# Performance work log

Hardware: AMD Instinct MI355X
Metric: run time of the kernel (lower is better)

The kernel has to match this reference:

```python
import jax, jax.numpy as jnp
import numpy as np

N = 100000   # nodes
E = 1200000  # edges
D = 64       # feature dim (in_channels == out_channels)


def gcn_layer(x, W, src, dst):
    # GCNConv(normalize=False, bias=False, aggr='add'):
    # linear transform then scatter-add of source messages into targets.
    h = x @ W                                            # [N, D]
    msg = h[src]                                         # [E, D] gather
    return jax.ops.segment_sum(msg, dst, num_segments=x.shape[0])  # [N, D]


def setup_inputs() -> dict:
    key = jax.random.key(0)
    ks = jax.random.split(key, 5)
    x = jax.random.normal(ks[0], (N, D), dtype=jnp.float32)
    edge_index = jax.random.randint(ks[1], (2, E), 0, N, dtype=jnp.int64)
    scale = 1.0 / np.sqrt(D).astype(np.float32)
    W0 = jax.random.normal(ks[2], (D, D), dtype=jnp.float32) * scale
    W1 = jax.random.normal(ks[3], (D, D), dtype=jnp.float32) * scale
    W2 = jax.random.normal(ks[4], (D, D), dtype=jnp.float32) * scale
    return {"x": x, "edge_index": edge_index, "W0": W0, "W1": W1, "W2": W2}


def reference(x, edge_index, W0, W1, W2):
    src = edge_index[0]  # messages flow source -> target (PyG default)
    dst = edge_index[1]
    # num_hop = 3 stacked convs; dropout p=0 and use_bn=False are no-ops.
    for W in (W0, W1, W2):
        x = gcn_layer(x, W, src, dst)
    return x
```

## Files before the change

### kernel.cpp

```cpp
#include <hip/hip_runtime.h>


#define GCN_D 64
#define SEGSHIFT 8
#define SEGROWS 256
#define MAXSEG 512
#define A_EPB 4096

typedef unsigned short ushort;

__device__ __forceinline__ float bf2f(ushort u) {
    union { unsigned u; float f; } c; c.u = ((unsigned)u) << 16; return c.f;
}
__device__ __forceinline__ ushort f2bf(float f) {
    union { float f; unsigned u; } c; c.f = f;
    const unsigned r = 0x7FFFu + ((c.u >> 16) & 1u);
    return (ushort)((c.u + r) >> 16);
}

__global__ __launch_bounds__(256) void k_wchain(const float* __restrict__ W0,
                                                const float* __restrict__ W1,
                                                const float* __restrict__ W2,
                                                float* __restrict__ Wc) {
    __shared__ float A[4096], B[4096], T[4096];
    const int t = threadIdx.x;
    for (int i = t; i < 1024; i += 256) {
        ((float4*)A)[i] = ((const float4*)W0)[i];
        ((float4*)B)[i] = ((const float4*)W1)[i];
    }
    __syncthreads();
#pragma unroll
    for (int g = 0; g < 4; ++g) {
        const int idx = t + 256 * g;
        const int r = idx >> 4, c4 = idx & 15;
        float4 acc = make_float4(0.f, 0.f, 0.f, 0.f);
#pragma unroll
        for (int k = 0; k < 64; ++k) {
            const float a = A[r * 64 + k];
            const float4 b = ((float4*)B)[k * 16 + c4];
            acc.x = fmaf(a, b.x, acc.x); acc.y = fmaf(a, b.y, acc.y);
            acc.z = fmaf(a, b.z, acc.z); acc.w = fmaf(a, b.w, acc.w);
        }
        ((float4*)T)[idx] = acc;
    }
    __syncthreads();
    for (int i = t; i < 1024; i += 256) ((float4*)B)[i] = ((const float4*)W2)[i];
    __syncthreads();
#pragma unroll
    for (int g = 0; g < 4; ++g) {
        const int idx = t + 256 * g;
        const int r = idx >> 4, c4 = idx & 15;
        float4 acc = make_float4(0.f, 0.f, 0.f, 0.f);
#pragma unroll
        for (int k = 0; k < 64; ++k) {
            const float a = T[r * 64 + k];
            const float4 b = ((float4*)B)[k * 16 + c4];
            acc.x = fmaf(a, b.x, acc.x); acc.y = fmaf(a, b.y, acc.y);
            acc.z = fmaf(a, b.z, acc.z); acc.w = fmaf(a, b.w, acc.w);
        }
        ((float4*)Wc)[idx] = acc;
    }
}

__global__ __launch_bounds__(256) void k_tobf(const float* __restrict__ X,
                                              ushort* __restrict__ B, long long n4) {
    const long long stride = (long long)gridDim.x * 256;
    for (long long i = blockIdx.x * 256ll + threadIdx.x; i < n4; i += stride) {
        const float4 v = ((const float4*)X)[i];
        ushort4 u;
        u.x = f2bf(v.x); u.y = f2bf(v.y); u.z = f2bf(v.z); u.w = f2bf(v.w);
        ((ushort4*)B)[i] = u;
    }
}

__global__ __launch_bounds__(256) void k_a0(const int* __restrict__ ei,
                                            int* __restrict__ ghist, int E) {
    __shared__ int h[MAXSEG];
    const int t = threadIdx.x;
    for (int i = t; i < MAXSEG; i += 256) h[i] = 0;
    __syncthreads();
    for (int e = blockIdx.x * 256 + t; e < E; e += gridDim.x * 256)
        atomicAdd(&h[ei[E + e] >> SEGSHIFT], 1);
    __syncthreads();
    for (int i = t; i < MAXSEG; i += 256) {
        const int c = h[i];
        if (c) atomicAdd(&ghist[i], c);
    }
}

__global__ __launch_bounds__(MAXSEG) void k_ascan(const int* __restrict__ ghist,
                                                  int* __restrict__ gOff,
                                                  int* __restrict__ gcur,
                                                  int* __restrict__ rp, int N, int E) {
    __shared__ int sd[MAXSEG];
    const int t = threadIdx.x;
    const int v = ghist[t];
    sd[t] = v; __syncthreads();
    for (int off = 1; off < MAXSEG; off <<= 1) {
        const int y = (t >= off) ? sd[t - off] : 0;
        __syncthreads();
        sd[t] += y;
        __syncthreads();
    }
    const int excl = sd[t] - v;
    gOff[t] = excl; gcur[t] = excl;
    if (t == MAXSEG - 1) gOff[MAXSEG] = sd[t];
    if (t == 0) rp[N] = E;
}

__global__ __launch_bounds__(512) void k_apart(const int* __restrict__ ei,
                                               int* __restrict__ gcur,
                                               uint2* __restrict__ ebuf, int E) {
    __shared__ int hist[MAXSEG], lofs[MAXSEG], cur[MAXSEG], gbase[MAXSEG];
    __shared__ uint2 stg[A_EPB];
    const int t = threadIdx.x;
    const int base = blockIdx.x * A_EPB;
    const int cnt = min(A_EPB, E - base);

    hist[t] = 0;
    __syncthreads();

    uint2 my[8]; int mb[8];
#pragma unroll
    for (int j = 0; j < 8; ++j) {
        const int i = t + j * 512;
        if (i < cnt) {
            const int e = base + i;
            const int s = ei[e];
            const int d = ei[E + e];
            my[j] = make_uint2((unsigned)s, (unsigned)d);
            mb[j] = d >> SEGSHIFT;
            atomicAdd(&hist[mb[j]], 1);
        } else mb[j] = -1;
    }
    __syncthreads();

    {
        const int v = hist[t];
        lofs[t] = v; __syncthreads();
        for (int off = 1; off < MAXSEG; off <<= 1) {
            const int y = (t >= off) ? lofs[t - off] : 0;
            __syncthreads();
            lofs[t] += y;
            __syncthreads();
        }
        const int excl = lofs[t] - v;
        __syncthreads();
        lofs[t] = excl; cur[t] = excl;
    }
    __syncthreads();

#pragma unroll
    for (int j = 0; j < 8; ++j) {
        if (mb[j] >= 0) {
            const int p = atomicAdd(&cur[mb[j]], 1);
            stg[p] = my[j];
        }
    }
    __syncthreads();

    {
        const int c = hist[t];
        gbase[t] = c ? atomicAdd(&gcur[t], c) : 0;
    }
    __syncthreads();

    for (int i = t; i < cnt; i += 512) {
        const uint2 pr = stg[i];
        const int b = (int)(pr.y >> SEGSHIFT);
        ebuf[(size_t)gbase[b] + (unsigned)(i - lofs[b])] = pr;
    }
}

__global__ __launch_bounds__(SEGROWS) void k_bplace(const uint2* __restrict__ ebuf,
                                                    const int* __restrict__ gOff,
                                                    int* __restrict__ rp,
                                                    int* __restrict__ cs, int N) {
    __shared__ int h[SEGROWS], ofs[SEGROWS];
    const int s = blockIdx.x;
    const int t = threadIdx.x;
    const int e0 = gOff[s];
    const int e1 = gOff[s + 1];

    h[t] = 0; __syncthreads();
    for (int e = e0 + t; e < e1; e += SEGROWS)
        atomicAdd(&h[ebuf[e].y & (SEGROWS - 1)], 1);
    __syncthreads();

    const int v = h[t];
    ofs[t] = v; __syncthreads();
    for (int off = 1; off < SEGROWS; off <<= 1) {
        const int y = (t >= off) ? ofs[t - off] : 0;
        __syncthreads();
        ofs[t] += y;
        __syncthreads();
    }
    const int excl = ofs[t] - v;
    const int r = s * SEGROWS + t;
    if (r < N) rp[r] = e0 + excl;
    __syncthreads();
    ofs[t] = excl;
    __syncthreads();

    for (int e = e0 + t; e < e1; e += SEGROWS) {
        const uint2 pr = ebuf[e];
        const int lr = (int)(pr.y & (SEGROWS - 1));
        const int p = atomicAdd(&ofs[lr], 1);
        cs[e0 + p] = (int)pr.x;
    }
}

__global__ __launch_bounds__(256) void k_aggc(const ushort* __restrict__ B,
                                              const int* __restrict__ rp,
                                              const int* __restrict__ cs,
                                              ushort* __restrict__ out, int N) {
    const int t = threadIdx.x;
    const int gw = (blockIdx.x * 256 + t) >> 6;
    const int lane = t & 63;
    const int q = lane >> 4;
    const int f4 = lane & 15;
    const int r = gw * 4 + q;
    if (r >= N) return;

    const int e0 = rp[r];
    const int e1 = rp[r + 1];
    const ushort4* Bv = (const ushort4*)B;

    float4 acc = make_float4(0.f, 0.f, 0.f, 0.f);
    int e = e0;
    for (; e + 3 < e1; e += 4) {
        const int s0 = cs[e], s1 = cs[e + 1], s2 = cs[e + 2], s3 = cs[e + 3];
        const ushort4 u0 = Bv[(size_t)s0 * 16 + f4];
        const ushort4 u1 = Bv[(size_t)s1 * 16 + f4];
        const ushort4 u2 = Bv[(size_t)s2 * 16 + f4];
        const ushort4 u3 = Bv[(size_t)s3 * 16 + f4];
        acc.x += bf2f(u0.x) + bf2f(u1.x) + bf2f(u2.x) + bf2f(u3.x);
        acc.y += bf2f(u0.y) + bf2f(u1.y) + bf2f(u2.y) + bf2f(u3.y);
        acc.z += bf2f(u0.z) + bf2f(u1.z) + bf2f(u2.z) + bf2f(u3.z);
        acc.w += bf2f(u0.w) + bf2f(u1.w) + bf2f(u2.w) + bf2f(u3.w);
    }
    for (; e < e1; ++e) {
        const ushort4 u = Bv[(size_t)cs[e] * 16 + f4];
        acc.x += bf2f(u.x); acc.y += bf2f(u.y);
        acc.z += bf2f(u.z); acc.w += bf2f(u.w);
    }
    ushort4 o;
    o.x = f2bf(acc.x); o.y = f2bf(acc.y); o.z = f2bf(acc.z); o.w = f2bf(acc.w);
    ((ushort4*)out)[(size_t)r * 16 + f4] = o;
}

__global__ __launch_bounds__(256) void gcn_gemm64b(const ushort* __restrict__ X,
                                                   const float* __restrict__ W,
                                                   float* __restrict__ H,
                                                   int nrows) {
    __shared__ float Wl[64 * 64];
    __shared__ float Xl[16][65];

    const int tid = threadIdx.x;
    for (int i = tid; i < 1024; i += 256) ((float4*)Wl)[i] = ((const float4*)W)[i];

    const int rowBase = blockIdx.x * 16;
    const int lr = tid >> 4;
    const int lc = tid & 15;
    const int grow = rowBase + lr;

    if (grow < nrows) {
        const ushort4 u = ((const ushort4*)X)[(size_t)grow * 16 + lc];
        Xl[lr][lc * 4 + 0] = bf2f(u.x);
        Xl[lr][lc * 4 + 1] = bf2f(u.y);
        Xl[lr][lc * 4 + 2] = bf2f(u.z);
        Xl[lr][lc * 4 + 3] = bf2f(u.w);
    }
    __syncthreads();

    float4 acc = make_float4(0.f, 0.f, 0.f, 0.f);
#pragma unroll
    for (int k = 0; k < 64; ++k) {
        const float xv = Xl[lr][k];
        const float4 w4 = ((const float4*)Wl)[k * 16 + lc];
        acc.x = fmaf(xv, w4.x, acc.x);
        acc.y = fmaf(xv, w4.y, acc.y);
        acc.z = fmaf(xv, w4.z, acc.z);
        acc.w = fmaf(xv, w4.w, acc.w);
    }
    if (grow < nrows) ((float4*)H)[(size_t)grow * 16 + lc] = acc;
}

__global__ __launch_bounds__(256) void gcn_gemm64(const float* __restrict__ X,
                                                  const float* __restrict__ W,
                                                  float* __restrict__ H,
                                                  int nrows) {
    __shared__ float Wl[64 * 64];
    __shared__ float Xl[16][65];
    const int tid = threadIdx.x;
    for (int i = tid; i < 1024; i += 256) ((float4*)Wl)[i] = ((const float4*)W)[i];
    const int rowBase = blockIdx.x * 16;
    const int lr = tid >> 4;
    const int lc = tid & 15;
    const int grow = rowBase + lr;
    if (grow < nrows) {
        float4 xv = ((const float4*)X)[(long long)grow * 16 + lc];
        Xl[lr][lc * 4 + 0] = xv.x; Xl[lr][lc * 4 + 1] = xv.y;
        Xl[lr][lc * 4 + 2] = xv.z; Xl[lr][lc * 4 + 3] = xv.w;
    }
    __syncthreads();
    float4 acc = make_float4(0.f, 0.f, 0.f, 0.f);
#pragma unroll
    for (int k = 0; k < 64; ++k) {
        const float xv = Xl[lr][k];
        const float4 w4 = ((const float4*)Wl)[k * 16 + lc];
        acc.x = fmaf(xv, w4.x, acc.x); acc.y = fmaf(xv, w4.y, acc.y);
        acc.z = fmaf(xv, w4.z, acc.z); acc.w = fmaf(xv, w4.w, acc.w);
    }
    if (grow < nrows) ((float4*)H)[(long long)grow * 16 + lc] = acc;
}

__global__ __launch_bounds__(256) void gcn_scatter(const float* __restrict__ H,
                                                   const int* __restrict__ ei,
                                                   float* __restrict__ out,
                                                   int nedges) {
    const long long t = (long long)blockIdx.x * 256 + threadIdx.x;
    const int e = (int)(t >> 4);
    if (e >= nedges) return;
    const int lc = (int)(t & 15);
    const int s = ei[e];
    const int d = ei[nedges + e];
    const float4 v = ((const float4*)H)[(long long)s * 16 + lc];
    float* o = out + (long long)d * GCN_D + lc * 4;
    atomicAdd(o + 0, v.x);
    atomicAdd(o + 1, v.y);
    atomicAdd(o + 2, v.z);
    atomicAdd(o + 3, v.w);
}

extern "C" void kernel_launch(void* const* d_in, const int* in_sizes, int n_in,
                              void* d_out, int out_size, void* d_ws, size_t ws_size,
                              hipStream_t stream) {
    const float* x  = (const float*)d_in[0];
    const int*   ei = (const int*)d_in[1];
    const float* W0 = (const float*)d_in[2];
    const float* W1 = (const float*)d_in[3];
    const float* W2 = (const float*)d_in[4];
    float* out = (float*)d_out;

    const int N_ = in_sizes[0] / GCN_D;
    const int E_ = in_sizes[1] / 2;
    const int NSEG = (N_ + SEGROWS - 1) >> SEGSHIFT;

    uintptr_t base = (uintptr_t)d_ws;
    ushort* B0 = (ushort*)base;
    const size_t bfBytes  = (size_t)N_ * GCN_D * 2;
    const size_t regBytes = bfBytes > (size_t)E_ * 8 ? bfBytes : (size_t)E_ * 8;
    ushort* B1   = (ushort*)(base + bfBytes);
    uint2*  ebuf = (uint2*)B1;
    int* rp    = (int*)(base + bfBytes + regBytes);
    int* gOff  = rp + (N_ + 2);
    int* ghist = gOff + (MAXSEG + 1);
    int* gcur  = ghist + MAXSEG;
    float* Wc  = (float*)(gcur + MAXSEG);
    int* cs    = (int*)(Wc + 4096);
    const size_t needed = ((uintptr_t)(cs + E_) - base);

    const int gemmBlocks = (N_ + 15) / 16;

    if (NSEG <= MAXSEG && ws_size >= needed) {
        k_wchain<<<1, 256, 0, stream>>>(W0, W1, W2, Wc);
        k_tobf<<<1024, 256, 0, stream>>>(x, B0, (long long)N_ * 16);
        hipMemsetAsync(ghist, 0, MAXSEG * 4, stream);
        k_a0<<<512, 256, 0, stream>>>(ei, ghist, E_);
        k_ascan<<<1, MAXSEG, 0, stream>>>(ghist, gOff, gcur, rp, N_, E_);
        k_apart<<<(E_ + A_EPB - 1) / A_EPB, 512, 0, stream>>>(ei, gcur, ebuf, E_);
        k_bplace<<<NSEG, SEGROWS, 0, stream>>>(ebuf, gOff, rp, cs, N_);

        const int aggBlocks = (N_ + 15) / 16;
        k_aggc<<<aggBlocks, 256, 0, stream>>>(B0, rp, cs, B1, N_);
        k_aggc<<<aggBlocks, 256, 0, stream>>>(B1, rp, cs, B0, N_);
        k_aggc<<<aggBlocks, 256, 0, stream>>>(B0, rp, cs, B1, N_);
        gcn_gemm64b<<<gemmBlocks, 256, 0, stream>>>(B1, Wc, out, N_);
    } else {
        float* h = (float*)d_ws;
        const int scatBlocks = (int)(((long long)E_ * 16 + 255) / 256);
        const int edgeBlocks = (E_ + 255) / 256;
        (void)edgeBlocks;
        const float* curAct = x;
        for (int l = 0; l < 3; ++l) {
            const float* Wl = (l == 0) ? W0 : (l == 1) ? W1 : W2;
            gcn_gemm64<<<gemmBlocks, 256, 0, stream>>>(curAct, Wl, h, N_);
            hipMemsetAsync(out, 0, (size_t)N_ * GCN_D * sizeof(float), stream);
            gcn_scatter<<<scatBlocks, 256, 0, stream>>>(h, ei, out, E_);
            curAct = out;
        }
    }
}
```

Measured before the change: 189.5 us.

## Fuse final aggregation with weight GEMM, pack edge pairs, unroll gathers

The last aggregation pass is merged with the dense 64x64 weight multiply, so the bf16 intermediate is no longer written out and read back by a separate GEMM kernel. Edge (src, dst) pairs in the partition buffer are packed into one 32-bit word (src<<8 | local row), which halves staging and buffer traffic. Because the destination is no longer stored, each element finds its bucket by binary search over the local offsets. The ghist memset is folded into the bf16 conversion kernel, and the gather loops are unrolled to 8 edges to keep more loads in flight. The packing only holds for N < 2^24, so a guard is added.

```diff
diff --git a/kernel.cpp b/kernel.cpp
--- a/kernel.cpp
+++ b/kernel.cpp
@@ -63,7 +63,11 @@
 }
 
 __global__ __launch_bounds__(256) void k_tobf(const float* __restrict__ X,
-                                              ushort* __restrict__ B, long long n4) {
+                                              ushort* __restrict__ B,
+                                              int* __restrict__ ghist, long long n4) {
+    if (blockIdx.x == 0) {
+        for (int i = threadIdx.x; i < MAXSEG; i += 256) ghist[i] = 0;
+    }
     const long long stride = (long long)gridDim.x * 256;
     for (long long i = blockIdx.x * 256ll + threadIdx.x; i < n4; i += stride) {
         const float4 v = ((const float4*)X)[i];
@@ -110,9 +114,9 @@
 
 __global__ __launch_bounds__(512) void k_apart(const int* __restrict__ ei,
                                                int* __restrict__ gcur,
-                                               uint2* __restrict__ ebuf, int E) {
+                                               unsigned* __restrict__ ebuf, int E) {
     __shared__ int hist[MAXSEG], lofs[MAXSEG], cur[MAXSEG], gbase[MAXSEG];
-    __shared__ uint2 stg[A_EPB];
+    __shared__ unsigned stg[A_EPB];
     const int t = threadIdx.x;
     const int base = blockIdx.x * A_EPB;
     const int cnt = min(A_EPB, E - base);
@@ -120,16 +124,16 @@
     hist[t] = 0;
     __syncthreads();
 
-    uint2 my[8]; int mb[8];
+    unsigned my[8]; int mb[8];
 #pragma unroll
     for (int j = 0; j < 8; ++j) {
         const int i = t + j * 512;
         if (i < cnt) {
             const int e = base + i;
-            const int s = ei[e];
-            const int d = ei[E + e];
-            my[j] = make_uint2((unsigned)s, (unsigned)d);
-            mb[j] = d >> SEGSHIFT;
+            const unsigned s = (unsigned)ei[e];
+            const unsigned d = (unsigned)ei[E + e];
+            my[j] = (s << 8) | (d & (SEGROWS - 1));
+            mb[j] = (int)(d >> SEGSHIFT);
             atomicAdd(&hist[mb[j]], 1);
         } else mb[j] = -1;
     }
@@ -166,13 +170,16 @@
     __syncthreads();
 
     for (int i = t; i < cnt; i += 512) {
-        const uint2 pr = stg[i];
-        const int b = (int)(pr.y >> SEGSHIFT);
-        ebuf[(size_t)gbase[b] + (unsigned)(i - lofs[b])] = pr;
-    }
-}
-
-__global__ __launch_bounds__(SEGROWS) void k_bplace(const uint2* __restrict__ ebuf,
+        int lo = 0, hi = MAXSEG - 1;
+        while (lo < hi) {
+            const int mid = (lo + hi + 1) >> 1;
+            if (lofs[mid] <= i) lo = mid; else hi = mid - 1;
+        }
+        ebuf[(size_t)gbase[lo] + (unsigned)(i - lofs[lo])] = stg[i];
+    }
+}
+
+__global__ __launch_bounds__(SEGROWS) void k_bplace(const unsigned* __restrict__ ebuf,
                                                     const int* __restrict__ gOff,
                                                     int* __restrict__ rp,
                                                     int* __restrict__ cs, int N) {
@@ -184,7 +191,7 @@
 
     h[t] = 0; __syncthreads();
     for (int e = e0 + t; e < e1; e += SEGROWS)
-        atomicAdd(&h[ebuf[e].y & (SEGROWS - 1)], 1);
+        atomicAdd(&h[ebuf[e] & (SEGROWS - 1)], 1);
     __syncthreads();
 
     const int v = h[t];
@@ -203,10 +210,10 @@
     __syncthreads();
 
     for (int e = e0 + t; e < e1; e += SEGROWS) {
-        const uint2 pr = ebuf[e];
-        const int lr = (int)(pr.y & (SEGROWS - 1));
+        const unsigned pr = ebuf[e];
+        const int lr = (int)(pr & (SEGROWS - 1));
         const int p = atomicAdd(&ofs[lr], 1);
-        cs[e0 + p] = (int)pr.x;
+        cs[e0 + p] = (int)(pr >> 8);
     }
 }
 
@@ -217,9 +224,8 @@
     const int t = threadIdx.x;
     const int gw = (blockIdx.x * 256 + t) >> 6;
     const int lane = t & 63;
-    const int q = lane >> 4;
     const int f4 = lane & 15;
-    const int r = gw * 4 + q;
+    const int r = gw * 4 + (lane >> 4);
     if (r >= N) return;
 
     const int e0 = rp[r];
@@ -228,16 +234,25 @@
 
     float4 acc = make_float4(0.f, 0.f, 0.f, 0.f);
     int e = e0;
+    for (; e + 7 < e1; e += 8) {
+        ushort4 u[8];
+#pragma unroll
+        for (int j = 0; j < 8; ++j) u[j] = Bv[(size_t)cs[e + j] * 16 + f4];
+#pragma unroll
+        for (int j = 0; j < 8; ++j) {
+            acc.x += bf2f(u[j].x); acc.y += bf2f(u[j].y);
+            acc.z += bf2f(u[j].z); acc.w += bf2f(u[j].w);
+        }
+    }
     for (; e + 3 < e1; e += 4) {
-        const int s0 = cs[e], s1 = cs[e + 1], s2 = cs[e + 2], s3 = cs[e + 3];
-        const ushort4 u0 = Bv[(size_t)s0 * 16 + f4];
-        const ushort4 u1 = Bv[(size_t)s1 * 16 + f4];
-        const ushort4 u2 = Bv[(size_t)s2 * 16 + f4];
-        const ushort4 u3 = Bv[(size_t)s3 * 16 + f4];
-        acc.x += bf2f(u0.x) + bf2f(u1.x) + bf2f(u2.x) + bf2f(u3.x);
-        acc.y += bf2f(u0.y) + bf2f(u1.y) + bf2f(u2.y) + bf2f(u3.y);
-        acc.z += bf2f(u0.z) + bf2f(u1.z) + bf2f(u2.z) + bf2f(u3.z);
-        acc.w += bf2f(u0.w) + bf2f(u1.w) + bf2f(u2.w) + bf2f(u3.w);
+        ushort4 u[4];
+#pragma unroll
+        for (int j = 0; j < 4; ++j) u[j] = Bv[(size_t)cs[e + j] * 16 + f4];
+#pragma unroll
+        for (int j = 0; j < 4; ++j) {
+            acc.x += bf2f(u[j].x); acc.y += bf2f(u[j].y);
+            acc.z += bf2f(u[j].z); acc.w += bf2f(u[j].w);
+        }
     }
     for (; e < e1; ++e) {
         const ushort4 u = Bv[(size_t)cs[e] * 16 + f4];
@@ -249,41 +264,67 @@
     ((ushort4*)out)[(size_t)r * 16 + f4] = o;
 }
 
-__global__ __launch_bounds__(256) void gcn_gemm64b(const ushort* __restrict__ X,
-                                                   const float* __restrict__ W,
-                                                   float* __restrict__ H,
-                                                   int nrows) {
+__global__ __launch_bounds__(256) void k_aggf(const ushort* __restrict__ B,
+                                              const int* __restrict__ rp,
+                                              const int* __restrict__ cs,
+                                              const float* __restrict__ Wc,
+                                              float* __restrict__ out, int N) {
     __shared__ float Wl[64 * 64];
     __shared__ float Xl[16][65];
-
-    const int tid = threadIdx.x;
-    for (int i = tid; i < 1024; i += 256) ((float4*)Wl)[i] = ((const float4*)W)[i];
-
-    const int rowBase = blockIdx.x * 16;
-    const int lr = tid >> 4;
-    const int lc = tid & 15;
-    const int grow = rowBase + lr;
-
-    if (grow < nrows) {
-        const ushort4 u = ((const ushort4*)X)[(size_t)grow * 16 + lc];
-        Xl[lr][lc * 4 + 0] = bf2f(u.x);
-        Xl[lr][lc * 4 + 1] = bf2f(u.y);
-        Xl[lr][lc * 4 + 2] = bf2f(u.z);
-        Xl[lr][lc * 4 + 3] = bf2f(u.w);
-    }
-    __syncthreads();
+    const int t = threadIdx.x;
+    for (int i = t; i < 1024; i += 256) ((float4*)Wl)[i] = ((const float4*)Wc)[i];
+
+    const int lr = t >> 4;
+    const int f4 = t & 15;
+    const int r = blockIdx.x * 16 + lr;
 
     float4 acc = make_float4(0.f, 0.f, 0.f, 0.f);
+    if (r < N) {
+        const int e0 = rp[r];
+        const int e1 = rp[r + 1];
+        const ushort4* Bv = (const ushort4*)B;
+        int e = e0;
+        for (; e + 7 < e1; e += 8) {
+            ushort4 u[8];
+#pragma unroll
+            for (int j = 0; j < 8; ++j) u[j] = Bv[(size_t)cs[e + j] * 16 + f4];
+#pragma unroll
+            for (int j = 0; j < 8; ++j) {
+                acc.x += bf2f(u[j].x); acc.y += bf2f(u[j].y);
+                acc.z += bf2f(u[j].z); acc.w += bf2f(u[j].w);
+            }
+        }
+        for (; e + 3 < e1; e += 4) {
+            ushort4 u[4];
+#pragma unroll
+            for (int j = 0; j < 4; ++j) u[j] = Bv[(size_t)cs[e + j] * 16 + f4];
+#pragma unroll
+            for (int j = 0; j < 4; ++j) {
+                acc.x += bf2f(u[j].x); acc.y += bf2f(u[j].y);
+                acc.z += bf2f(u[j].z); acc.w += bf2f(u[j].w);
+            }
+        }
+        for (; e < e1; ++e) {
+            const ushort4 u = Bv[(size_t)cs[e] * 16 + f4];
+            acc.x += bf2f(u.x); acc.y += bf2f(u.y);
+            acc.z += bf2f(u.z); acc.w += bf2f(u.w);
+        }
+    }
+    Xl[lr][f4 * 4 + 0] = bf2f(f2bf(acc.x));
+    Xl[lr][f4 * 4 + 1] = bf2f(f2bf(acc.y));
+    Xl[lr][f4 * 4 + 2] = bf2f(f2bf(acc.z));
+    Xl[lr][f4 * 4 + 3] = bf2f(f2bf(acc.w));
+    __syncthreads();
+
+    float4 g = make_float4(0.f, 0.f, 0.f, 0.f);
 #pragma unroll
     for (int k = 0; k < 64; ++k) {
         const float xv = Xl[lr][k];
-        const float4 w4 = ((const float4*)Wl)[k * 16 + lc];
-        acc.x = fmaf(xv, w4.x, acc.x);
-        acc.y = fmaf(xv, w4.y, acc.y);
-        acc.z = fmaf(xv, w4.z, acc.z);
-        acc.w = fmaf(xv, w4.w, acc.w);
-    }
-    if (grow < nrows) ((float4*)H)[(size_t)grow * 16 + lc] = acc;
+        const float4 w4 = ((const float4*)Wl)[k * 16 + f4];
+        g.x = fmaf(xv, w4.x, g.x); g.y = fmaf(xv, w4.y, g.y);
+        g.z = fmaf(xv, w4.z, g.z); g.w = fmaf(xv, w4.w, g.w);
+    }
+    if (r < N) ((float4*)out)[(size_t)r * 16 + f4] = g;
 }
 
 __global__ __launch_bounds__(256) void gcn_gemm64(const float* __restrict__ X,
@@ -308,7 +349,7 @@
 #pragma unroll
     for (int k = 0; k < 64; ++k) {
         const float xv = Xl[lr][k];
-        const float4 w4 = ((const float4*)Wl)[k * 16 + lc];
+        const float4 w4 = ((float4*)Wl)[k * 16 + lc];
         acc.x = fmaf(xv, w4.x, acc.x); acc.y = fmaf(xv, w4.y, acc.y);
         acc.z = fmaf(xv, w4.z, acc.z); acc.w = fmaf(xv, w4.w, acc.w);
     }
@@ -350,9 +391,9 @@
     uintptr_t base = (uintptr_t)d_ws;
     ushort* B0 = (ushort*)base;
     const size_t bfBytes  = (size_t)N_ * GCN_D * 2;
-    const size_t regBytes = bfBytes > (size_t)E_ * 8 ? bfBytes : (size_t)E_ * 8;
-    ushort* B1   = (ushort*)(base + bfBytes);
-    uint2*  ebuf = (uint2*)B1;
+    const size_t regBytes = bfBytes > (size_t)E_ * 4 ? bfBytes : (size_t)E_ * 4;
+    ushort*   B1   = (ushort*)(base + bfBytes);
+    unsigned* ebuf = (unsigned*)B1;
     int* rp    = (int*)(base + bfBytes + regBytes);
     int* gOff  = rp + (N_ + 2);
     int* ghist = gOff + (MAXSEG + 1);
@@ -363,10 +404,9 @@
 
     const int gemmBlocks = (N_ + 15) / 16;
 
-    if (NSEG <= MAXSEG && ws_size >= needed) {
+    if (NSEG <= MAXSEG && N_ < (1 << 24) && ws_size >= needed) {
         k_wchain<<<1, 256, 0, stream>>>(W0, W1, W2, Wc);
-        k_tobf<<<1024, 256, 0, stream>>>(x, B0, (long long)N_ * 16);
-        hipMemsetAsync(ghist, 0, MAXSEG * 4, stream);
+        k_tobf<<<1024, 256, 0, stream>>>(x, B0, ghist, (long long)N_ * 16);
         k_a0<<<512, 256, 0, stream>>>(ei, ghist, E_);
         k_ascan<<<1, MAXSEG, 0, stream>>>(ghist, gOff, gcur, rp, N_, E_);
         k_apart<<<(E_ + A_EPB - 1) / A_EPB, 512, 0, stream>>>(ei, gcur, ebuf, E_);
@@ -375,13 +415,10 @@
         const int aggBlocks = (N_ + 15) / 16;
         k_aggc<<<aggBlocks, 256, 0, stream>>>(B0, rp, cs, B1, N_);
         k_aggc<<<aggBlocks, 256, 0, stream>>>(B1, rp, cs, B0, N_);
-        k_aggc<<<aggBlocks, 256, 0, stream>>>(B0, rp, cs, B1, N_);
-        gcn_gemm64b<<<gemmBlocks, 256, 0, stream>>>(B1, Wc, out, N_);
+        k_aggf<<<aggBlocks, 256, 0, stream>>>(B0, rp, cs, Wc, out, N_);
     } else {
         float* h = (float*)d_ws;
         const int scatBlocks = (int)(((long long)E_ * 16 + 255) / 256);
-        const int edgeBlocks = (E_ + 255) / 256;
-        (void)edgeBlocks;
         const float* curAct = x;
         for (int l = 0; l < 3; ++l) {
             const float* Wl = (l == 0) ? W0 : (l == 1) ? W1 : W2;
```

Result: faster. 177.1 us (-6.5%).
